# Performance work log

Hardware: AMD Instinct MI355X
Metric: run time of the kernel (lower is better)

## Reference

```python
import jax, jax.numpy as jnp
import numpy as np

EPS = 1e-5  # BatchNorm eps


def setup_inputs() -> dict:
    key = jax.random.key(0)
    ks = jax.random.split(key, 13)
    B, C, H, W = 8, 256, 64, 64
    Ci = 128
    s = 0.05
    return {
        "x": jax.random.normal(ks[0], (B, C, H, W), jnp.float32),
        "Wt": jax.random.normal(ks[1], (Ci, C), jnp.float32) * s,
        "bt": jax.random.normal(ks[2], (Ci,), jnp.float32) * s,
        "Wp": jax.random.normal(ks[3], (Ci, C), jnp.float32) * s,
        "bp": jax.random.normal(ks[4], (Ci,), jnp.float32) * s,
        "Wg": jax.random.normal(ks[5], (Ci, C), jnp.float32) * s,
        "bg": jax.random.normal(ks[6], (Ci,), jnp.float32) * s,
        "Wz": jax.random.normal(ks[7], (C, Ci), jnp.float32) * s,
        "bz": jax.random.normal(ks[8], (C,), jnp.float32) * s,
        "gamma": jax.random.normal(ks[9], (C,), jnp.float32) * s,
        "beta": jax.random.normal(ks[10], (C,), jnp.float32) * s,
        "rmean": jax.random.normal(ks[11], (C,), jnp.float32) * s,
        "rvar": jax.random.uniform(ks[12], (C,), jnp.float32, 0.5, 1.5),
    }


def reference(x, Wt, bt, Wp, bp, Wg, bg, Wz, bz, gamma, beta, rmean, rvar):
    B, C, H, W = x.shape
    N = H * W
    xf = x.reshape(B, C, N)                                  # [B,C,N]
    # 1x1 conv projections == channel GEMMs
    theta = jnp.einsum('oc,bcn->bno', Wt, xf) + bt           # [B,N,Ci]
    phi = jnp.einsum('oc,bcn->bon', Wp, xf) + bp[:, None]    # [B,Ci,N]
    g = jnp.einsum('oc,bcn->bno', Wg, xf) + bg               # [B,N,Ci]
    # single-head attention over all N=H*W positions
    attn = jax.nn.softmax(jnp.einsum('bnc,bcm->bnm', theta, phi), axis=-1)
    y = jnp.einsum('bnm,bmc->bnc', attn, g)                  # [B,N,Ci]
    # W_z: 1x1 conv + BatchNorm (eval mode: running stats) + residual
    z = jnp.einsum('oc,bnc->bon', Wz, y) + bz[:, None]       # [B,C,N]
    inv = gamma / jnp.sqrt(rvar + EPS)                       # [C]
    zn = (z - rmean[:, None]) * inv[:, None] + beta[:, None]
    return zn.reshape(B, C, H, W) + x
```

## Files before the change

kernel.cpp:

```cpp
#include <hip/hip_runtime.h>
#include <stdint.h>

typedef __attribute__((ext_vector_type(8))) short bf16x8;
typedef __attribute__((ext_vector_type(4))) float f32x4;
typedef __attribute__((ext_vector_type(16))) float f32x16;

__device__ __forceinline__ unsigned short f32_to_bf16(float f) {
  union { float f; uint32_t u; } v; v.f = f;
  uint32_t u = v.u;
  u += 0x7fffu + ((u >> 16) & 1u);
  return (unsigned short)(u >> 16);
}

__device__ __forceinline__ float bf16_to_f32(unsigned short s) {
  union { uint32_t u; float f; } v; v.u = ((uint32_t)s) << 16;
  return v.f;
}

__device__ __forceinline__ uint32_t cvt_pk_bf16(float a, float b) {
  uint32_t r;
  asm("v_cvt_pk_bf16_f32 %0, %1, %2" : "=v"(r) : "v"(a), "v"(b));
  return r;
}

__device__ __forceinline__ void async_copy16(void* lds, const void* g) {
  __builtin_amdgcn_global_load_lds(
      (const __attribute__((address_space(1))) unsigned int*)g,
      (__attribute__((address_space(3))) unsigned int*)lds, 16, 0, 0);
}

__global__ __launch_bounds__(256) void xpose_kernel(
    const float* __restrict__ x, unsigned short* __restrict__ xT) {
  __shared__ unsigned short ts[32][260];
  const int t = threadIdx.x;
  const int bid = blockIdx.x;
  const int b = bid >> 7;
  const int ct = (bid >> 4) & 7;
  const int nt = bid & 15;
  const int c0 = ct * 32, n0 = nt * 256;

  const float* xb = x + ((size_t)b * 256 + c0) * 4096 + n0;
#pragma unroll
  for (int i = 0; i < 8; ++i) {
    int flat = i * 256 + t;
    int c = flat >> 6, nq = flat & 63;
    float4 v = *(const float4*)(xb + (size_t)c * 4096 + nq * 4);
    union { uint2 u; unsigned short s[4]; } pk;
    pk.s[0] = f32_to_bf16(v.x); pk.s[1] = f32_to_bf16(v.y);
    pk.s[2] = f32_to_bf16(v.z); pk.s[3] = f32_to_bf16(v.w);
    *(uint2*)&ts[c][nq * 4] = pk.u;
  }
  __syncthreads();

  unsigned short* xo = xT + ((size_t)b * 4096 + n0) * 256 + c0;
#pragma unroll
  for (int i = 0; i < 4; ++i) {
    int flat = i * 256 + t;
    int n = flat >> 2, ch = flat & 3;
    union { uint4 u; unsigned short s[8]; } pk;
#pragma unroll
    for (int jj = 0; jj < 8; ++jj) pk.s[jj] = ts[ch * 8 + jj][n];
    *(uint4*)(xo + (size_t)n * 256 + ch * 8) = pk.u;
  }
}

__global__ __launch_bounds__(256) void wcvt_kernel(
    const float* __restrict__ Wt, const float* __restrict__ Wp,
    const float* __restrict__ Wg, const float* __restrict__ Wz,
    unsigned short* __restrict__ Wcat, unsigned short* __restrict__ Wzb) {
  int e = (blockIdx.x * 256 + threadIdx.x) * 4;
  const float* src;
  unsigned short* dst;
  int off;
  if (e < 32768) { src = Wt; dst = Wcat; off = e; }
  else if (e < 65536) { src = Wp; dst = Wcat + 32768; off = e - 32768; }
  else if (e < 98304) { src = Wg; dst = Wcat + 65536; off = e - 65536; }
  else { src = Wz; dst = Wzb; off = e - 98304; }
  float4 v = *(const float4*)(src + off);
  union { uint2 u; unsigned short s[4]; } pk;
  pk.s[0] = f32_to_bf16(v.x); pk.s[1] = f32_to_bf16(v.y);
  pk.s[2] = f32_to_bf16(v.z); pk.s[3] = f32_to_bf16(v.w);
  *(uint2*)(dst + off) = pk.u;
}

__global__ __launch_bounds__(512, 2) void proj_kernel(
    const unsigned short* __restrict__ xT,
    const unsigned short* __restrict__ Wcat,
    const float* __restrict__ bt, const float* __restrict__ bp,
    const float* __restrict__ bg,
    unsigned short* __restrict__ Q, unsigned short* __restrict__ Km,
    unsigned short* __restrict__ Vt) {
  __shared__ __align__(1024) unsigned short xs[128 * 256];
  const int t = threadIdx.x;
  const int lane = t & 63;
  const int w = t >> 6;
  const int nt = blockIdx.x;
  const int b = blockIdx.y;
  const int n0 = nt * 128;

  const unsigned char* xTb =
      (const unsigned char*)(xT + ((size_t)b * 4096 + n0) * 256);
  unsigned char* lbase = (unsigned char*)xs;
#pragma unroll
  for (int i = 0; i < 8; ++i) {
    int base = (w * 8 + i) * 1024;
    int off = base + lane * 16;
    int n = off >> 9;
    int bir = off & 511;
    async_copy16(lbase + base, xTb + n * 512 + (bir ^ ((n & 7) << 4)));
  }
  __syncthreads();

  const int rl = lane & 15, gh = lane >> 4;
  const int swz = (rl & 7) << 4;
  const int rlv = (rl & 3) | ((rl & 4) << 1) | ((rl & 8) >> 1);

  f32x4 aQ[8], aK[8], aV[8];
#pragma unroll
  for (int i = 0; i < 8; ++i) {
    aQ[i] = (f32x4){0.f, 0.f, 0.f, 0.f};
    aK[i] = (f32x4){0.f, 0.f, 0.f, 0.f};
    aV[i] = (f32x4){0.f, 0.f, 0.f, 0.f};
  }

  const unsigned char* wq =
      (const unsigned char*)Wcat + ((w * 16 + rl) * 256) * 2 + gh * 16;
  const unsigned char* wk = wq + 128 * 512;
  const unsigned char* wv = wq + 256 * 512;

#pragma unroll
  for (int kk = 0; kk < 8; ++kk) {
    bf16x8 xf[8];
#pragma unroll
    for (int n2 = 0; n2 < 8; ++n2)
      xf[n2] = *(const bf16x8*)(lbase + (n2 * 16 + rl) * 512 +
                                ((kk * 64 + gh * 16) ^ swz));
    bf16x8 fq = *(const bf16x8*)(wq + kk * 64);
    bf16x8 fk = *(const bf16x8*)(wk + kk * 64);
    bf16x8 fv = *(const bf16x8*)(wv + kk * 64);
#pragma unroll
    for (int n2 = 0; n2 < 8; ++n2) {
      aQ[n2] = __builtin_amdgcn_mfma_f32_16x16x32_bf16(xf[n2], fq, aQ[n2], 0, 0, 0);
      aK[n2] = __builtin_amdgcn_mfma_f32_16x16x32_bf16(xf[n2], fk, aK[n2], 0, 0, 0);
      aV[n2] = __builtin_amdgcn_mfma_f32_16x16x32_bf16(fv, xf[n2], aV[n2], 0, 0, 0);
    }
  }

  const float btv = bt[w * 16 + rl];
  const float bpv = bp[w * 16 + rl];
  float bgv[4];
#pragma unroll
  for (int j = 0; j < 4; ++j) bgv[j] = bg[w * 16 + gh * 4 + j];

  unsigned short* Qb = Q + ((size_t)b * 4096 + n0) * 128 + w * 16 + rl;
  unsigned short* Kb = Km + ((size_t)b * 4096 + n0) * 128 + w * 16 + rl;
  unsigned short* Vb = Vt + (size_t)b * 128 * 4096 + n0 + rlv;
#pragma unroll
  for (int n2 = 0; n2 < 8; ++n2) {
#pragma unroll
    for (int j = 0; j < 4; ++j) {
      int n = n2 * 16 + gh * 4 + j;
      Qb[(size_t)n * 128] = f32_to_bf16(aQ[n2][j] + btv);
      Kb[(size_t)n * 128] = f32_to_bf16(aK[n2][j] + bpv);
      int o = w * 16 + gh * 4 + j;
      Vb[(size_t)o * 4096 + n2 * 16] = f32_to_bf16(aV[n2][j] + bgv[j]);
    }
  }
}

__global__ __launch_bounds__(256, 2) void attn_kernel(
    const unsigned short* __restrict__ Qg,
    const unsigned short* __restrict__ Kg,
    const unsigned short* __restrict__ Vg,
    unsigned short* __restrict__ Opart,
    float* __restrict__ Marr, float* __restrict__ Larr) {
  __shared__ __align__(1024) unsigned char smem[65536];
  const int t = threadIdx.x;
  const int lane = t & 63;
  const int w = t >> 6;
  const int q31 = lane & 31;
  const int hi = lane >> 5;
  const int swz = (q31 & 7) << 4;

  const int orig = blockIdx.x;
  const int b = orig & 7;
  const int idx = orig >> 3;
  const int h = idx & 1;
  const int qg = idx >> 1;
  const int qw = qg * 128 + w * 32;
  const int kv0 = h * 2048;

  const unsigned short* Qb = Qg + (size_t)b * 4096 * 128;
  const unsigned short* Kb = Kg + (size_t)b * 4096 * 128;
  const unsigned short* Vb = Vg + (size_t)b * 128 * 4096;

  bf16x8 qf[8];
  {
    const unsigned char* qp =
        (const unsigned char*)(Qb + (size_t)(qw + q31) * 128) + hi * 16;
#pragma unroll
    for (int dc = 0; dc < 8; ++dc) qf[dc] = *(const bf16x8*)(qp + dc * 32);
  }

  const unsigned char* ksrc[4];
  const unsigned char* vsrc[4];
  unsigned int kofs[4], vofs[4];
#pragma unroll
  for (int ii = 0; ii < 4; ++ii) {
    int seg = w * 4 + ii;
    int r = seg * 4 + (lane >> 4);
    int co = ((lane & 15) * 16) ^ ((r & 7) << 4);
    ksrc[ii] = (const unsigned char*)(Kb + (size_t)(kv0 + r) * 128) + co;
    kofs[ii] = seg * 1024;
    int d = seg * 8 + (lane >> 3);
    int vo = ((lane & 7) * 16) ^ ((d & 7) << 4);
    vsrc[ii] = (const unsigned char*)(Vb + (size_t)d * 4096 + kv0) + vo;
    vofs[ii] = 16384 + seg * 1024;
  }

  f32x16 acc[4];
#pragma unroll
  for (int i = 0; i < 4; ++i)
#pragma unroll
    for (int e = 0; e < 16; ++e) acc[i][e] = 0.f;
  float m = -1e30f, l = 0.f;

#pragma unroll
  for (int ii = 0; ii < 4; ++ii) {
    async_copy16(smem + kofs[ii], ksrc[ii]);
    async_copy16(smem + vofs[ii], vsrc[ii]);
  }
  __syncthreads();

#pragma unroll 2
  for (int it = 0; it < 32; ++it) {
    unsigned char* bb = smem + (it & 1) * 32768;
    if (it + 1 < 32) {
      unsigned int nb = ((it + 1) & 1) * 32768;
      size_t ko = (size_t)(it + 1) * 16384;
      int vo2 = (it + 1) * 128;
#pragma unroll
      for (int ii = 0; ii < 4; ++ii) {
        async_copy16(smem + nb + kofs[ii], ksrc[ii] + ko);
        async_copy16(smem + nb + vofs[ii], vsrc[ii] + vo2);
      }
    }

    f32x16 st0, st1;
#pragma unroll
    for (int e = 0; e < 16; ++e) { st0[e] = 0.f; st1[e] = 0.f; }
    const unsigned char* kb0 = bb + q31 * 256;
    const unsigned char* kb1 = bb + (32 + q31) * 256;
    __builtin_amdgcn_s_setprio(1);
#pragma unroll
    for (int dc = 0; dc < 8; ++dc) {
      int off = (dc * 32 + hi * 16) ^ swz;
      bf16x8 k0 = *(const bf16x8*)(kb0 + off);
      bf16x8 k1 = *(const bf16x8*)(kb1 + off);
      st0 = __builtin_amdgcn_mfma_f32_32x32x16_bf16(k0, qf[dc], st0, 0, 0, 0);
      st1 = __builtin_amdgcn_mfma_f32_32x32x16_bf16(k1, qf[dc], st1, 0, 0, 0);
    }
    __builtin_amdgcn_s_setprio(0);

    float tmax = st0[0];
#pragma unroll
    for (int e = 1; e < 16; ++e) tmax = fmaxf(tmax, st0[e]);
#pragma unroll
    for (int e = 0; e < 16; ++e) tmax = fmaxf(tmax, st1[e]);
#pragma unroll
    for (int off = 1; off < 64; off <<= 1)
      tmax = fmaxf(tmax, __shfl_xor(tmax, off));
    if (tmax > m + 8.f) {
      float mn = fmaxf(m, tmax);
      float sc = __expf(m - mn);
      m = mn;
      l *= sc;
#pragma unroll
      for (int i = 0; i < 4; ++i)
#pragma unroll
        for (int e = 0; e < 16; ++e) acc[i][e] *= sc;
    }
    float ls = 0.f;
#pragma unroll
    for (int e = 0; e < 16; ++e) { st0[e] = __expf(st0[e] - m); ls += st0[e]; }
#pragma unroll
    for (int e = 0; e < 16; ++e) { st1[e] = __expf(st1[e] - m); ls += st1[e]; }
    l += ls;

    const unsigned char* vb0 = bb + 16384 + q31 * 128;
#pragma unroll
    for (int ks = 0; ks < 4; ++ks) {
      union { uint32_t u[4]; bf16x8 v; } pk;
      if (ks == 0) {
        pk.u[0] = cvt_pk_bf16(st0[0], st0[1]);
        pk.u[1] = cvt_pk_bf16(st0[2], st0[3]);
        pk.u[2] = cvt_pk_bf16(st0[4], st0[5]);
        pk.u[3] = cvt_pk_bf16(st0[6], st0[7]);
      } else if (ks == 1) {
        pk.u[0] = cvt_pk_bf16(st0[8], st0[9]);
        pk.u[1] = cvt_pk_bf16(st0[10], st0[11]);
        pk.u[2] = cvt_pk_bf16(st0[12], st0[13]);
        pk.u[3] = cvt_pk_bf16(st0[14], st0[15]);
      } else if (ks == 2) {
        pk.u[0] = cvt_pk_bf16(st1[0], st1[1]);
        pk.u[1] = cvt_pk_bf16(st1[2], st1[3]);
        pk.u[2] = cvt_pk_bf16(st1[4], st1[5]);
        pk.u[3] = cvt_pk_bf16(st1[6], st1[7]);
      } else {
        pk.u[0] = cvt_pk_bf16(st1[8], st1[9]);
        pk.u[1] = cvt_pk_bf16(st1[10], st1[11]);
        pk.u[2] = cvt_pk_bf16(st1[12], st1[13]);
        pk.u[3] = cvt_pk_bf16(st1[14], st1[15]);
      }
      __builtin_amdgcn_s_setprio(1);
#pragma unroll
      for (int dt = 0; dt < 4; ++dt) {
        bf16x8 vf = *(const bf16x8*)(vb0 + dt * 32 * 128 +
                                     ((ks * 32 + hi * 16) ^ swz));
        acc[dt] = __builtin_amdgcn_mfma_f32_32x32x16_bf16(pk.v, vf, acc[dt], 0, 0, 0);
      }
      __builtin_amdgcn_s_setprio(0);
    }
    __syncthreads();
  }

  float lf = l + __shfl_xor(l, 32);
  if (lane < 32) {
    size_t ix = (size_t)h * 32768 + (size_t)b * 4096 + qw + q31;
    Marr[ix] = m;
    Larr[ix] = lf;
  }
  unsigned short* ob = Opart + (size_t)h * 32768 * 128;
#pragma unroll
  for (int dt = 0; dt < 4; ++dt)
#pragma unroll
    for (int r = 0; r < 16; ++r) {
      int qrow = qw + (r & 3) + 8 * (r >> 2) + 4 * hi;
      ob[((size_t)b * 4096 + qrow) * 128 + dt * 32 + q31] =
          f32_to_bf16(acc[dt][r]);
    }
}

__global__ __launch_bounds__(256) void comb_kernel(
    const unsigned short* __restrict__ Opart,
    const float* __restrict__ Marr, const float* __restrict__ Larr,
    unsigned short* __restrict__ Y) {
  int i = blockIdx.x * 256 + threadIdx.x;
  int q = i >> 4;
  int d8 = (i & 15) * 8;
  float m0 = Marr[q], m1 = Marr[32768 + q];
  float l0 = Larr[q], l1 = Larr[32768 + q];
  float M = fmaxf(m0, m1);
  float e0 = __expf(m0 - M), e1 = __expf(m1 - M);
  float rl = 1.f / (e0 * l0 + e1 * l1);
  float f0 = e0 * rl, f1 = e1 * rl;
  const bf16x8 o0 = *(const bf16x8*)(Opart + (size_t)q * 128 + d8);
  const bf16x8 o1 =
      *(const bf16x8*)(Opart + 32768ull * 128 + (size_t)q * 128 + d8);
  union { uint4 u4; unsigned short s[8]; } pk;
#pragma unroll
  for (int e = 0; e < 8; ++e) {
    float v = f0 * bf16_to_f32((unsigned short)o0[e]) +
              f1 * bf16_to_f32((unsigned short)o1[e]);
    pk.s[e] = f32_to_bf16(v);
  }
  *(uint4*)(Y + (size_t)q * 128 + d8) = pk.u4;
}

__global__ __launch_bounds__(512, 2) void outz_kernel(
    const unsigned short* __restrict__ Y,
    const unsigned short* __restrict__ Wzb,
    const float* __restrict__ x, const float* __restrict__ bz,
    const float* __restrict__ gamma, const float* __restrict__ beta,
    const float* __restrict__ rmean, const float* __restrict__ rvar,
    float* __restrict__ out) {
  __shared__ __align__(1024) unsigned short ys[128 * 128];
  const int t = threadIdx.x;
  const int lane = t & 63;
  const int w = t >> 6;
  const int nt = blockIdx.x;
  const int b = blockIdx.y;
  const int n0 = nt * 128;

  const unsigned char* Yb =
      (const unsigned char*)(Y + ((size_t)b * 4096 + n0) * 128);
  unsigned char* lbase = (unsigned char*)ys;
#pragma unroll
  for (int i = 0; i < 4; ++i) {
    int base = (w * 4 + i) * 1024;
    int off = base + lane * 16;
    int n = off >> 8;
    int bir = off & 255;
    async_copy16(lbase + base, Yb + n * 256 + (bir ^ ((n & 7) << 4)));
  }
  __syncthreads();

  const int rl = lane & 15, gh = lane >> 4;
  const int swz = (rl & 7) << 4;

  f32x4 acc[2][8];
#pragma unroll
  for (int i = 0; i < 2; ++i)
#pragma unroll
    for (int j = 0; j < 8; ++j) acc[i][j] = (f32x4){0.f, 0.f, 0.f, 0.f};

  const unsigned char* wz0 =
      (const unsigned char*)Wzb + ((w * 2) * 16 + rl) * 256 + gh * 16;

#pragma unroll
  for (int kk = 0; kk < 4; ++kk) {
    bf16x8 yf[8];
#pragma unroll
    for (int n2 = 0; n2 < 8; ++n2)
      yf[n2] = *(const bf16x8*)(lbase + (n2 * 16 + rl) * 256 +
                                ((kk * 64 + gh * 16) ^ swz));
    bf16x8 f0 = *(const bf16x8*)(wz0 + kk * 64);
    bf16x8 f1 = *(const bf16x8*)(wz0 + 16 * 256 + kk * 64);
#pragma unroll
    for (int n2 = 0; n2 < 8; ++n2) {
      acc[0][n2] = __builtin_amdgcn_mfma_f32_16x16x32_bf16(f0, yf[n2], acc[0][n2], 0, 0, 0);
      acc[1][n2] = __builtin_amdgcn_mfma_f32_16x16x32_bf16(f1, yf[n2], acc[1][n2], 0, 0, 0);
    }
  }

#pragma unroll
  for (int ot = 0; ot < 2; ++ot) {
#pragma unroll
    for (int j = 0; j < 4; ++j) {
      int o = (w * 2 + ot) * 16 + gh * 4 + j;
      float scale = gamma[o] * rsqrtf(rvar[o] + 1e-5f);
      float shift = (bz[o] - rmean[o]) * scale + beta[o];
      const float* xr = x + ((size_t)b * 256 + o) * 4096 + n0;
      float* orow = out + ((size_t)b * 256 + o) * 4096 + n0;
#pragma unroll
      for (int n2 = 0; n2 < 8; ++n2) {
        int n = n2 * 16 + rl;
        orow[n] = acc[ot][n2][j] * scale + shift + xr[n];
      }
    }
  }
}

extern "C" void kernel_launch(void* const* d_in, const int* in_sizes, int n_in,
                              void* d_out, int out_size, void* d_ws,
                              size_t ws_size, hipStream_t stream) {
  const float* x     = (const float*)d_in[0];
  const float* Wt    = (const float*)d_in[1];
  const float* bt    = (const float*)d_in[2];
  const float* Wp    = (const float*)d_in[3];
  const float* bp    = (const float*)d_in[4];
  const float* Wg    = (const float*)d_in[5];
  const float* bg    = (const float*)d_in[6];
  const float* Wz    = (const float*)d_in[7];
  const float* bz    = (const float*)d_in[8];
  const float* gamma = (const float*)d_in[9];
  const float* beta  = (const float*)d_in[10];
  const float* rmean = (const float*)d_in[11];
  const float* rvar  = (const float*)d_in[12];
  float* out = (float*)d_out;

  const size_t NE = (size_t)8 * 4096 * 128;
  unsigned short* Wcat  = (unsigned short*)d_ws;
  unsigned short* Wzb   = Wcat + 98304;
  float*          Marr  = (float*)(Wzb + 32768);
  float*          Larr  = Marr + 65536;
  unsigned short* xT    = (unsigned short*)(Larr + 65536);
  unsigned short* Opart = xT;
  unsigned short* Q     = xT + 2 * NE;
  unsigned short* Km    = Q + NE;
  unsigned short* Vt    = Km + NE;
  unsigned short* Y     = Km;

  wcvt_kernel<<<128, 256, 0, stream>>>(Wt, Wp, Wg, Wz, Wcat, Wzb);
  xpose_kernel<<<1024, 256, 0, stream>>>(x, xT);
  proj_kernel<<<dim3(32, 8), 512, 0, stream>>>(xT, Wcat, bt, bp, bg, Q, Km, Vt);
  attn_kernel<<<512, 256, 0, stream>>>(Q, Km, Vt, Opart, Marr, Larr);
  comb_kernel<<<2048, 256, 0, stream>>>(Opart, Marr, Larr, Y);
  outz_kernel<<<dim3(32, 8), 512, 0, stream>>>(Y, Wzb, x, bz, gamma, beta,
                                               rmean, rvar, out);
}
```

Before: 141.2 us.

## Split attention KV into four chunks with smaller tiles and higher occupancy

The attention kernel is templated on the KV split count, and a four-way split is launched when workspace allows. This doubles the grid, and the KV tile shrinks from 64 to 32 rows per iteration, halving shared memory and allowing four blocks per CU. The combine kernel is generalized to merge N partial softmax results. In exchange, partial-output traffic and combine work grow, each block runs more barrier-bound iterations with less MFMA work per iteration, and the V layout in shared memory changes.

```diff
diff --git a/kernel.cpp b/kernel.cpp
--- a/kernel.cpp
+++ b/kernel.cpp
@@ -168,13 +168,16 @@
   }
 }
 
-__global__ __launch_bounds__(256, 2) void attn_kernel(
+template <int LOGSPLIT>
+__global__ __launch_bounds__(256, 4) void attn_kernel(
     const unsigned short* __restrict__ Qg,
     const unsigned short* __restrict__ Kg,
     const unsigned short* __restrict__ Vg,
     unsigned short* __restrict__ Opart,
     float* __restrict__ Marr, float* __restrict__ Larr) {
-  __shared__ __align__(1024) unsigned char smem[65536];
+  constexpr int NSPLIT = 1 << LOGSPLIT;
+  constexpr int ITERS = (4096 / NSPLIT) / 32;
+  __shared__ __align__(1024) unsigned char smem[32768];
   const int t = threadIdx.x;
   const int lane = t & 63;
   const int w = t >> 6;
@@ -185,10 +188,10 @@
   const int orig = blockIdx.x;
   const int b = orig & 7;
   const int idx = orig >> 3;
-  const int h = idx & 1;
-  const int qg = idx >> 1;
+  const int h = idx & (NSPLIT - 1);
+  const int qg = idx >> LOGSPLIT;
   const int qw = qg * 128 + w * 32;
-  const int kv0 = h * 2048;
+  const int kv0 = h * (4096 / NSPLIT);
 
   const unsigned short* Qb = Qg + (size_t)b * 4096 * 128;
   const unsigned short* Kb = Kg + (size_t)b * 4096 * 128;
@@ -202,20 +205,28 @@
     for (int dc = 0; dc < 8; ++dc) qf[dc] = *(const bf16x8*)(qp + dc * 32);
   }
 
-  const unsigned char* ksrc[4];
-  const unsigned char* vsrc[4];
-  unsigned int kofs[4], vofs[4];
-#pragma unroll
-  for (int ii = 0; ii < 4; ++ii) {
-    int seg = w * 4 + ii;
-    int r = seg * 4 + (lane >> 4);
-    int co = ((lane & 15) * 16) ^ ((r & 7) << 4);
-    ksrc[ii] = (const unsigned char*)(Kb + (size_t)(kv0 + r) * 128) + co;
-    kofs[ii] = seg * 1024;
-    int d = seg * 8 + (lane >> 3);
-    int vo = ((lane & 7) * 16) ^ ((d & 7) << 4);
-    vsrc[ii] = (const unsigned char*)(Vb + (size_t)d * 4096 + kv0) + vo;
-    vofs[ii] = 16384 + seg * 1024;
+  const unsigned char* ksrc[2];
+  const unsigned char* vsrc[2];
+  unsigned int kdst[2], vdst[2];
+#pragma unroll
+  for (int i = 0; i < 2; ++i) {
+    int s = i * 256 + t;
+    {
+      int o = s * 16;
+      int r = o >> 8;
+      int col = (o & 255) ^ ((r & 7) << 4);
+      ksrc[i] = (const unsigned char*)(Kb + (size_t)(kv0 + r) * 128) + col;
+      kdst[i] = o;
+    }
+    {
+      int o = s * 16;
+      int row = o >> 7;
+      int col = (o & 127) ^ ((row & 7) << 4);
+      int d = row * 2 + (col >> 6);
+      int kvv = (col & 63) >> 1;
+      vsrc[i] = (const unsigned char*)(Vb + (size_t)d * 4096 + kv0 + kvv);
+      vdst[i] = 8192 + o;
+    }
   }
 
   f32x16 acc[4];
@@ -226,47 +237,40 @@
   float m = -1e30f, l = 0.f;
 
 #pragma unroll
-  for (int ii = 0; ii < 4; ++ii) {
-    async_copy16(smem + kofs[ii], ksrc[ii]);
-    async_copy16(smem + vofs[ii], vsrc[ii]);
+  for (int i = 0; i < 2; ++i) {
+    async_copy16(smem + kdst[i], ksrc[i]);
+    async_copy16(smem + vdst[i], vsrc[i]);
   }
   __syncthreads();
 
-#pragma unroll 2
-  for (int it = 0; it < 32; ++it) {
-    unsigned char* bb = smem + (it & 1) * 32768;
-    if (it + 1 < 32) {
-      unsigned int nb = ((it + 1) & 1) * 32768;
-      size_t ko = (size_t)(it + 1) * 16384;
-      int vo2 = (it + 1) * 128;
-#pragma unroll
-      for (int ii = 0; ii < 4; ++ii) {
-        async_copy16(smem + nb + kofs[ii], ksrc[ii] + ko);
-        async_copy16(smem + nb + vofs[ii], vsrc[ii] + vo2);
+  for (int it = 0; it < ITERS; ++it) {
+    unsigned char* bb = smem + (it & 1) * 16384;
+    if (it + 1 < ITERS) {
+      unsigned int nb = ((it + 1) & 1) * 16384;
+      size_t ko = (size_t)(it + 1) * 8192;
+      int vo = (it + 1) * 64;
+#pragma unroll
+      for (int i = 0; i < 2; ++i) {
+        async_copy16(smem + nb + kdst[i], ksrc[i] + ko);
+        async_copy16(smem + nb + vdst[i], vsrc[i] + vo);
       }
     }
 
-    f32x16 st0, st1;
-#pragma unroll
-    for (int e = 0; e < 16; ++e) { st0[e] = 0.f; st1[e] = 0.f; }
+    f32x16 st0;
+#pragma unroll
+    for (int e = 0; e < 16; ++e) st0[e] = 0.f;
     const unsigned char* kb0 = bb + q31 * 256;
-    const unsigned char* kb1 = bb + (32 + q31) * 256;
     __builtin_amdgcn_s_setprio(1);
 #pragma unroll
     for (int dc = 0; dc < 8; ++dc) {
-      int off = (dc * 32 + hi * 16) ^ swz;
-      bf16x8 k0 = *(const bf16x8*)(kb0 + off);
-      bf16x8 k1 = *(const bf16x8*)(kb1 + off);
+      bf16x8 k0 = *(const bf16x8*)(kb0 + ((dc * 32 + hi * 16) ^ swz));
       st0 = __builtin_amdgcn_mfma_f32_32x32x16_bf16(k0, qf[dc], st0, 0, 0, 0);
-      st1 = __builtin_amdgcn_mfma_f32_32x32x16_bf16(k1, qf[dc], st1, 0, 0, 0);
     }
     __builtin_amdgcn_s_setprio(0);
 
     float tmax = st0[0];
 #pragma unroll
     for (int e = 1; e < 16; ++e) tmax = fmaxf(tmax, st0[e]);
-#pragma unroll
-    for (int e = 0; e < 16; ++e) tmax = fmaxf(tmax, st1[e]);
 #pragma unroll
     for (int off = 1; off < 64; off <<= 1)
       tmax = fmaxf(tmax, __shfl_xor(tmax, off));
@@ -283,40 +287,30 @@
     float ls = 0.f;
 #pragma unroll
     for (int e = 0; e < 16; ++e) { st0[e] = __expf(st0[e] - m); ls += st0[e]; }
-#pragma unroll
-    for (int e = 0; e < 16; ++e) { st1[e] = __expf(st1[e] - m); ls += st1[e]; }
     l += ls;
 
-    const unsigned char* vb0 = bb + 16384 + q31 * 128;
-#pragma unroll
-    for (int ks = 0; ks < 4; ++ks) {
+    const unsigned char* vb = bb + 8192 + ((q31 >> 1) * 128);
+    const int vx = (q31 & 1) * 64;
+    const int vswz = ((q31 >> 1) & 7) << 4;
+#pragma unroll
+    for (int ks = 0; ks < 2; ++ks) {
       union { uint32_t u[4]; bf16x8 v; } pk;
       if (ks == 0) {
         pk.u[0] = cvt_pk_bf16(st0[0], st0[1]);
         pk.u[1] = cvt_pk_bf16(st0[2], st0[3]);
         pk.u[2] = cvt_pk_bf16(st0[4], st0[5]);
         pk.u[3] = cvt_pk_bf16(st0[6], st0[7]);
-      } else if (ks == 1) {
+      } else {
         pk.u[0] = cvt_pk_bf16(st0[8], st0[9]);
         pk.u[1] = cvt_pk_bf16(st0[10], st0[11]);
         pk.u[2] = cvt_pk_bf16(st0[12], st0[13]);
         pk.u[3] = cvt_pk_bf16(st0[14], st0[15]);
-      } else if (ks == 2) {
-        pk.u[0] = cvt_pk_bf16(st1[0], st1[1]);
-        pk.u[1] = cvt_pk_bf16(st1[2], st1[3]);
-        pk.u[2] = cvt_pk_bf16(st1[4], st1[5]);
-        pk.u[3] = cvt_pk_bf16(st1[6], st1[7]);
-      } else {
-        pk.u[0] = cvt_pk_bf16(st1[8], st1[9]);
-        pk.u[1] = cvt_pk_bf16(st1[10], st1[11]);
-        pk.u[2] = cvt_pk_bf16(st1[12], st1[13]);
-        pk.u[3] = cvt_pk_bf16(st1[14], st1[15]);
       }
       __builtin_amdgcn_s_setprio(1);
 #pragma unroll
       for (int dt = 0; dt < 4; ++dt) {
-        bf16x8 vf = *(const bf16x8*)(vb0 + dt * 32 * 128 +
-                                     ((ks * 32 + hi * 16) ^ swz));
+        bf16x8 vf = *(const bf16x8*)(vb + dt * 16 * 128 +
+                                     ((vx + ks * 32 + hi * 16) ^ vswz));
         acc[dt] = __builtin_amdgcn_mfma_f32_32x32x16_bf16(pk.v, vf, acc[dt], 0, 0, 0);
       }
       __builtin_amdgcn_s_setprio(0);
@@ -341,6 +335,7 @@
     }
 }
 
+template <int NSPLIT>
 __global__ __launch_bounds__(256) void comb_kernel(
     const unsigned short* __restrict__ Opart,
     const float* __restrict__ Marr, const float* __restrict__ Larr,
@@ -348,22 +343,36 @@
   int i = blockIdx.x * 256 + threadIdx.x;
   int q = i >> 4;
   int d8 = (i & 15) * 8;
-  float m0 = Marr[q], m1 = Marr[32768 + q];
-  float l0 = Larr[q], l1 = Larr[32768 + q];
-  float M = fmaxf(m0, m1);
-  float e0 = __expf(m0 - M), e1 = __expf(m1 - M);
-  float rl = 1.f / (e0 * l0 + e1 * l1);
-  float f0 = e0 * rl, f1 = e1 * rl;
-  const bf16x8 o0 = *(const bf16x8*)(Opart + (size_t)q * 128 + d8);
-  const bf16x8 o1 =
-      *(const bf16x8*)(Opart + 32768ull * 128 + (size_t)q * 128 + d8);
+  float mv[NSPLIT], lv[NSPLIT];
+  float M = -1e30f;
+#pragma unroll
+  for (int s = 0; s < NSPLIT; ++s) {
+    mv[s] = Marr[s * 32768 + q];
+    lv[s] = Larr[s * 32768 + q];
+    M = fmaxf(M, mv[s]);
+  }
+  float fs[NSPLIT];
+  float denom = 0.f;
+#pragma unroll
+  for (int s = 0; s < NSPLIT; ++s) {
+    fs[s] = __expf(mv[s] - M);
+    denom += fs[s] * lv[s];
+  }
+  float rd = 1.f / denom;
+  float o[8];
+#pragma unroll
+  for (int e = 0; e < 8; ++e) o[e] = 0.f;
+#pragma unroll
+  for (int s = 0; s < NSPLIT; ++s) {
+    const bf16x8 os =
+        *(const bf16x8*)(Opart + (size_t)s * 32768 * 128 + (size_t)q * 128 + d8);
+#pragma unroll
+    for (int e = 0; e < 8; ++e)
+      o[e] += fs[s] * bf16_to_f32((unsigned short)os[e]);
+  }
   union { uint4 u4; unsigned short s[8]; } pk;
 #pragma unroll
-  for (int e = 0; e < 8; ++e) {
-    float v = f0 * bf16_to_f32((unsigned short)o0[e]) +
-              f1 * bf16_to_f32((unsigned short)o1[e]);
-    pk.s[e] = f32_to_bf16(v);
-  }
+  for (int e = 0; e < 8; ++e) pk.s[e] = f32_to_bf16(o[e] * rd);
   *(uint4*)(Y + (size_t)q * 128 + d8) = pk.u4;
 }
 
@@ -463,19 +472,28 @@
   unsigned short* Wcat  = (unsigned short*)d_ws;
   unsigned short* Wzb   = Wcat + 98304;
   float*          Marr  = (float*)(Wzb + 32768);
-  float*          Larr  = Marr + 65536;
-  unsigned short* xT    = (unsigned short*)(Larr + 65536);
-  unsigned short* Opart = xT;
+  float*          Larr  = Marr + 4 * 32768;
+  unsigned short* xT    = (unsigned short*)(Larr + 4 * 32768);
   unsigned short* Q     = xT + 2 * NE;
   unsigned short* Km    = Q + NE;
   unsigned short* Vt    = Km + NE;
+  unsigned short* Obig  = Vt + NE;
   unsigned short* Y     = Km;
+
+  const size_t need4 = (size_t)((char*)(Obig + 4 * NE) - (char*)d_ws);
+  const bool big = ws_size >= need4;
 
   wcvt_kernel<<<128, 256, 0, stream>>>(Wt, Wp, Wg, Wz, Wcat, Wzb);
   xpose_kernel<<<1024, 256, 0, stream>>>(x, xT);
   proj_kernel<<<dim3(32, 8), 512, 0, stream>>>(xT, Wcat, bt, bp, bg, Q, Km, Vt);
-  attn_kernel<<<512, 256, 0, stream>>>(Q, Km, Vt, Opart, Marr, Larr);
-  comb_kernel<<<2048, 256, 0, stream>>>(Opart, Marr, Larr, Y);
+  if (big) {
+    attn_kernel<2><<<1024, 256, 0, stream>>>(Q, Km, Vt, Obig, Marr, Larr);
+    comb_kernel<4><<<2048, 256, 0, stream>>>(Obig, Marr, Larr, Y);
+  } else {
+    unsigned short* Opart = xT;
+    attn_kernel<1><<<512, 256, 0, stream>>>(Q, Km, Vt, Opart, Marr, Larr);
+    comb_kernel<2><<<2048, 256, 0, stream>>>(Opart, Marr, Larr, Y);
+  }
   outz_kernel<<<dim3(32, 8), 512, 0, stream>>>(Y, Wzb, x, bz, gamma, beta,
                                                rmean, rvar, out);
 }
```

Result: slower. 183.2 us (+29.7%).

## Widen LDS swizzle for K/V tiles and read bf16 residual copy in output

Applied to the files above, without the earlier changes.

The attention kernel's K tile swizzle changes from an XOR over 8 rows to one over 16 rows. The V tile is repacked so two d-rows share a 256-byte LDS line with a matching XOR swizzle, which should cut bank conflicts on the LDS reads that feed the MFMAs. Separately, the transpose kernel now also writes a bf16 copy of x in channel-major order, and the output kernel reads that instead of the fp32 x for the residual add. This halves residual read traffic but adds an extra write pass and rounds the residual to bf16, which costs accuracy.

```diff
diff --git a/kernel.cpp b/kernel.cpp
--- a/kernel.cpp
+++ b/kernel.cpp
@@ -30,7 +30,8 @@
 }
 
 __global__ __launch_bounds__(256) void xpose_kernel(
-    const float* __restrict__ x, unsigned short* __restrict__ xT) {
+    const float* __restrict__ x, unsigned short* __restrict__ xT,
+    unsigned short* __restrict__ xc) {
   __shared__ unsigned short ts[32][260];
   const int t = threadIdx.x;
   const int bid = blockIdx.x;
@@ -49,6 +50,7 @@
     pk.s[0] = f32_to_bf16(v.x); pk.s[1] = f32_to_bf16(v.y);
     pk.s[2] = f32_to_bf16(v.z); pk.s[3] = f32_to_bf16(v.w);
     *(uint2*)&ts[c][nq * 4] = pk.u;
+    *(uint2*)(xc + ((size_t)b * 256 + c0 + c) * 4096 + n0 + nq * 4) = pk.u;
   }
   __syncthreads();
 
@@ -180,7 +182,7 @@
   const int w = t >> 6;
   const int q31 = lane & 31;
   const int hi = lane >> 5;
-  const int swz = (q31 & 7) << 4;
+  const int kswz = (q31 & 15) << 4;
 
   const int orig = blockIdx.x;
   const int b = orig & 7;
@@ -208,14 +210,21 @@
 #pragma unroll
   for (int ii = 0; ii < 4; ++ii) {
     int seg = w * 4 + ii;
-    int r = seg * 4 + (lane >> 4);
-    int co = ((lane & 15) * 16) ^ ((r & 7) << 4);
-    ksrc[ii] = (const unsigned char*)(Kb + (size_t)(kv0 + r) * 128) + co;
-    kofs[ii] = seg * 1024;
-    int d = seg * 8 + (lane >> 3);
-    int vo = ((lane & 7) * 16) ^ ((d & 7) << 4);
-    vsrc[ii] = (const unsigned char*)(Vb + (size_t)d * 4096 + kv0) + vo;
-    vofs[ii] = 16384 + seg * 1024;
+    {
+      int r = seg * 4 + (lane >> 4);
+      int kcol = ((lane & 15) * 16) ^ ((r & 15) << 4);
+      ksrc[ii] = (const unsigned char*)(Kb + (size_t)(kv0 + r) * 128) + kcol;
+      kofs[ii] = seg * 1024;
+    }
+    {
+      int o = seg * 1024 + lane * 16;
+      int R = o >> 8;
+      int cp = (o & 255) ^ ((R & 15) << 4);
+      int d = 2 * R + (cp >> 7);
+      int kvb = cp & 127;
+      vsrc[ii] = (const unsigned char*)(Vb + (size_t)d * 4096 + kv0) + kvb;
+      vofs[ii] = 16384 + seg * 1024;
+    }
   }
 
   f32x16 acc[4];
@@ -254,7 +263,7 @@
     __builtin_amdgcn_s_setprio(1);
 #pragma unroll
     for (int dc = 0; dc < 8; ++dc) {
-      int off = (dc * 32 + hi * 16) ^ swz;
+      int off = (dc * 32 + hi * 16) ^ kswz;
       bf16x8 k0 = *(const bf16x8*)(kb0 + off);
       bf16x8 k1 = *(const bf16x8*)(kb1 + off);
       st0 = __builtin_amdgcn_mfma_f32_32x32x16_bf16(k0, qf[dc], st0, 0, 0, 0);
@@ -287,7 +296,9 @@
     for (int e = 0; e < 16; ++e) { st1[e] = __expf(st1[e] - m); ls += st1[e]; }
     l += ls;
 
-    const unsigned char* vb0 = bb + 16384 + q31 * 128;
+    const unsigned char* vbase = bb + 16384 + (q31 >> 1) * 256;
+    const int vhb = (q31 & 1) << 7;
+    const int vswz = (q31 >> 1) << 4;
 #pragma unroll
     for (int ks = 0; ks < 4; ++ks) {
       union { uint32_t u[4]; bf16x8 v; } pk;
@@ -315,8 +326,8 @@
       __builtin_amdgcn_s_setprio(1);
 #pragma unroll
       for (int dt = 0; dt < 4; ++dt) {
-        bf16x8 vf = *(const bf16x8*)(vb0 + dt * 32 * 128 +
-                                     ((ks * 32 + hi * 16) ^ swz));
+        bf16x8 vf = *(const bf16x8*)(
+            vbase + dt * 4096 + ((vhb | (ks * 32 + hi * 16)) ^ vswz));
         acc[dt] = __builtin_amdgcn_mfma_f32_32x32x16_bf16(pk.v, vf, acc[dt], 0, 0, 0);
       }
       __builtin_amdgcn_s_setprio(0);
@@ -370,7 +381,7 @@
 __global__ __launch_bounds__(512, 2) void outz_kernel(
     const unsigned short* __restrict__ Y,
     const unsigned short* __restrict__ Wzb,
-    const float* __restrict__ x, const float* __restrict__ bz,
+    const unsigned short* __restrict__ xc, const float* __restrict__ bz,
     const float* __restrict__ gamma, const float* __restrict__ beta,
     const float* __restrict__ rmean, const float* __restrict__ rvar,
     float* __restrict__ out) {
@@ -430,12 +441,12 @@
       int o = (w * 2 + ot) * 16 + gh * 4 + j;
       float scale = gamma[o] * rsqrtf(rvar[o] + 1e-5f);
       float shift = (bz[o] - rmean[o]) * scale + beta[o];
-      const float* xr = x + ((size_t)b * 256 + o) * 4096 + n0;
+      const unsigned short* xr = xc + ((size_t)b * 256 + o) * 4096 + n0;
       float* orow = out + ((size_t)b * 256 + o) * 4096 + n0;
 #pragma unroll
       for (int n2 = 0; n2 < 8; ++n2) {
         int n = n2 * 16 + rl;
-        orow[n] = acc[ot][n2][j] * scale + shift + xr[n];
+        orow[n] = acc[ot][n2][j] * scale + shift + bf16_to_f32(xr[n]);
       }
     }
   }
@@ -463,19 +474,20 @@
   unsigned short* Wcat  = (unsigned short*)d_ws;
   unsigned short* Wzb   = Wcat + 98304;
   float*          Marr  = (float*)(Wzb + 32768);
-  float*          Larr  = Marr + 65536;
-  unsigned short* xT    = (unsigned short*)(Larr + 65536);
-  unsigned short* Opart = xT;
+  float*          Larr  = Marr + 2 * 32768;
+  unsigned short* xT    = (unsigned short*)(Larr + 2 * 32768);
   unsigned short* Q     = xT + 2 * NE;
   unsigned short* Km    = Q + NE;
   unsigned short* Vt    = Km + NE;
+  unsigned short* xc    = Vt + NE;
+  unsigned short* Opart = xT;
   unsigned short* Y     = Km;
 
   wcvt_kernel<<<128, 256, 0, stream>>>(Wt, Wp, Wg, Wz, Wcat, Wzb);
-  xpose_kernel<<<1024, 256, 0, stream>>>(x, xT);
+  xpose_kernel<<<1024, 256, 0, stream>>>(x, xT, xc);
   proj_kernel<<<dim3(32, 8), 512, 0, stream>>>(xT, Wcat, bt, bp, bg, Q, Km, Vt);
   attn_kernel<<<512, 256, 0, stream>>>(Q, Km, Vt, Opart, Marr, Larr);
   comb_kernel<<<2048, 256, 0, stream>>>(Opart, Marr, Larr, Y);
-  outz_kernel<<<dim3(32, 8), 512, 0, stream>>>(Y, Wzb, x, bz, gamma, beta,
+  outz_kernel<<<dim3(32, 8), 512, 0, stream>>>(Y, Wzb, xc, bz, gamma, beta,
                                                rmean, rvar, out);
 }
```

Result: faster. 137.9 us (-2.3%).
